# Kernel optimization log

Measured on AMD Instinct MI355X. Metric: run time of the kernel, lower is better.

Reference implementation:

```python
import jax, jax.numpy as jnp
import numpy as np
from math import factorial

# (mul, l, parity) per irrep; parity +1 = even (e), -1 = odd (o)
IRREPS_IN  = [(64, 0, 1), (32, 1, -1), (16, 2, 1)]
IRREPS_OUT = [(64, 0, 1), (32, 1, -1), (16, 2, 1)]
B = 20000


def _su2_cg(j1, m1, j2, m2, j3, m3):
    # Standard SU(2) Clebsch-Gordan coefficient <j1 m1 j2 m2 | j3 m3> (integer j).
    if m3 != m1 + m2:
        return 0.0
    vmin = max(-j1 + j2 + m3, -j1 + m1, 0)
    vmax = min(j2 + j3 + m1, j3 - j1 + j2, j3 + m3)
    if vmax < vmin:
        return 0.0
    f = factorial
    C = ((2 * j3 + 1) * f(j3 + j1 - j2) * f(j3 - j1 + j2) * f(j1 + j2 - j3)
         * f(j3 + m3) * f(j3 - m3)
         / (f(j1 + j2 + j3 + 1) * f(j1 - m1) * f(j1 + m1) * f(j2 - m2) * f(j2 + m2))) ** 0.5
    S = 0.0
    for v in range(vmin, vmax + 1):
        S += ((-1.0) ** (v + j2 + m2) * f(j2 + j3 + m1 - v) * f(j1 - m1 + v)
              / (f(v) * f(j3 - j1 + j2 - v) * f(j3 + m3 - v) * f(v + j1 - j2 - m3)))
    return C * S


def _q(l):
    # Real -> complex spherical-harmonics change of basis, phased so real CG is real (e3nn convention).
    q = np.zeros((2 * l + 1, 2 * l + 1), dtype=np.complex128)
    for m in range(-l, 0):
        q[l + m, l + abs(m)] = 2 ** -0.5
        q[l + m, l - abs(m)] = -1j * 2 ** -0.5
    q[l, l] = 1.0
    for m in range(1, l + 1):
        q[l + m, l + abs(m)] = (-1) ** m * 2 ** -0.5
        q[l + m, l - abs(m)] = 1j * (-1) ** m * 2 ** -0.5
    return (-1j) ** l * q


def _clebsch_gordan(l1, l2, l3):
    # Real-basis CG coefficients, shape (2l1+1, 2l2+1, 2l3+1).
    C = np.zeros((2 * l1 + 1, 2 * l2 + 1, 2 * l3 + 1), dtype=np.complex128)
    for m1 in range(-l1, l1 + 1):
        for m2 in range(-l2, l2 + 1):
            for m3 in range(-l3, l3 + 1):
                C[l1 + m1, l2 + m2, l3 + m3] = _su2_cg(l1, m1, l2, m2, l3, m3)
    Q1, Q2, Q3 = _q(l1), _q(l2), _q(l3)
    Cr = np.einsum('ij,kl,mn,ikn->jlm', Q1, Q2, np.conj(Q3.T), C)
    return np.real(Cr)


def _build():
    # Enumerate all allowed 'uvw' CG paths (i1, i2, i_out); one learned weight per path.
    ins, cgs = [], []
    for i1, (m1, l1, p1) in enumerate(IRREPS_IN):
        for i2, (m2, l2, p2) in enumerate(IRREPS_IN):
            for lo in range(abs(l1 - l2), l1 + l2 + 1):
                po = p1 * p2
                for io, (mo, l3, p3) in enumerate(IRREPS_OUT):
                    if l3 == lo and p3 == po:
                        ins.append((i1, i2, io, (m1, m2, mo)))
                        # 'component' normalization: scale so each output component has unit variance per path
                        cgs.append((_clebsch_gordan(l1, l2, l3) * (2 * l3 + 1) ** 0.5).astype(np.float32))
                        break
    fan = {}
    for (i1, i2, io, (m1, m2, mo)) in ins:
        fan[io] = fan.get(io, 0) + m1 * m2
    alphas = [1.0 / float(np.sqrt(fan[io])) for (_, _, io, _) in ins]
    return ins, cgs, alphas


INSTRUCTIONS, CGS, ALPHAS = _build()  # 11 instructions for these irreps
DIM_IN = sum(m * (2 * l + 1) for m, l, _ in IRREPS_IN)


def setup_inputs() -> dict:
    key = jax.random.key(0)
    keys = jax.random.split(key, 1 + len(INSTRUCTIONS))
    inp = {"x": jax.random.normal(keys[0], (B, DIM_IN), dtype=jnp.float32)}
    for i, (ins, k) in enumerate(zip(INSTRUCTIONS, keys[1:])):
        inp[f"w{i}"] = jax.random.normal(k, ins[3], dtype=jnp.float32)
    return inp


def _tensor_square(x, ws):
    b = x.shape[0]
    xs, off = [], 0
    for m, l, _ in IRREPS_IN:
        d = m * (2 * l + 1)
        xs.append(x[:, off:off + d].reshape(b, m, 2 * l + 1))
        off += d
    outs = [jnp.zeros((b, m, 2 * l + 1), x.dtype) for m, l, _ in IRREPS_OUT]
    for (i1, i2, io, _), w, C, a in zip(INSTRUCTIONS, ws, CGS, ALPHAS):
        # per-path weighted CG contraction: out[b,w,k] = sum_{u,v,i,j} W[u,v,w] C[i,j,k] x[b,u,i] x[b,v,j]
        contrib = jnp.einsum('uvw,ijk,bui,bvj->bwk', w, jnp.asarray(C, x.dtype),
                             xs[i1], xs[i2], optimize='optimal')
        outs[io] = outs[io] + jnp.asarray(a, x.dtype) * contrib
    return jnp.concatenate([o.reshape(b, -1) for o in outs], axis=1)


def reference(x, w0, w1, w2, w3, w4, w5, w6, w7, w8, w9, w10):
    return _tensor_square(x, (w0, w1, w2, w3, w4, w5, w6, w7, w8, w9, w10))
```

## Files before the change

kernel.cpp:

```cpp
#include <hip/hip_runtime.h>
#include <stdint.h>
#include <stddef.h>


namespace cg {

struct Cx { double re, im; };
constexpr Cx cmul(Cx a, Cx b){ return { a.re*b.re - a.im*b.im, a.re*b.im + a.im*b.re }; }

constexpr double fact(int n){ double r = 1.0; for (int i = 2; i <= n; ++i) r *= (double)i; return r; }

constexpr double csqrt(double x){
  if (x <= 0.0) return 0.0;
  double r = x > 1.0 ? x : 1.0;
  for (int i = 0; i < 50; ++i) r = 0.5*(r + x/r);
  return r;
}

constexpr double neg1pow(int k){ return (k % 2 == 0) ? 1.0 : -1.0; }

constexpr double su2_cg(int j1,int m1,int j2,int m2,int j3,int m3){
  if (m3 != m1 + m2) return 0.0;
  int vmin = -j1 + j2 + m3;
  if (-j1 + m1 > vmin) vmin = -j1 + m1;
  if (0 > vmin) vmin = 0;
  int vmax = j2 + j3 + m1;
  if (j3 - j1 + j2 < vmax) vmax = j3 - j1 + j2;
  if (j3 + m3 < vmax) vmax = j3 + m3;
  if (vmax < vmin) return 0.0;
  double C = csqrt((2.0*j3 + 1.0)*fact(j3+j1-j2)*fact(j3-j1+j2)*fact(j1+j2-j3)
                   *fact(j3+m3)*fact(j3-m3)
                   /(fact(j1+j2+j3+1)*fact(j1-m1)*fact(j1+m1)*fact(j2-m2)*fact(j2+m2)));
  double S = 0.0;
  for (int v = vmin; v <= vmax; ++v)
    S += neg1pow(v + j2 + m2)*fact(j2+j3+m1-v)*fact(j1-m1+v)
       /(fact(v)*fact(j3-j1+j2-v)*fact(j3+m3-v)*fact(v+j1-j2-m3));
  return C*S;
}

struct QM { Cx v[5][5]; };
constexpr QM qmat(int l){
  QM q{};
  const double r2 = 0.70710678118654752440;
  for (int m = -l; m < 0; ++m){
    q.v[l+m][l-m] = Cx{ r2, 0.0 };
    q.v[l+m][l+m] = Cx{ 0.0, -r2 };
  }
  q.v[l][l] = Cx{ 1.0, 0.0 };
  for (int m = 1; m <= l; ++m){
    double s = neg1pow(m)*r2;
    q.v[l+m][l+m] = Cx{ s, 0.0 };
    q.v[l+m][l-m] = Cx{ 0.0, s };
  }
  Cx ph = (l % 4 == 0) ? Cx{1,0} : (l % 4 == 1) ? Cx{0,-1} : (l % 4 == 2) ? Cx{-1,0} : Cx{0,1};
  QM out{};
  for (int i = 0; i < 5; ++i) for (int j = 0; j < 5; ++j) out.v[i][j] = cmul(ph, q.v[i][j]);
  return out;
}

struct CGT { double v[5][5][5]; };
constexpr CGT cg_tab(int l1,int l2,int l3){
  double C[5][5][5] = {};
  for (int m1 = -l1; m1 <= l1; ++m1)
    for (int m2 = -l2; m2 <= l2; ++m2)
      for (int m3 = -l3; m3 <= l3; ++m3)
        C[l1+m1][l2+m2][l3+m3] = su2_cg(l1,m1,l2,m2,l3,m3);
  QM Q1 = qmat(l1), Q2 = qmat(l2), Q3 = qmat(l3);
  const int n1 = 2*l1+1, n2 = 2*l2+1, n3 = 2*l3+1;
  const double norm = csqrt(2.0*l3 + 1.0);
  CGT R{};
  for (int j = 0; j < n1; ++j)
    for (int l = 0; l < n2; ++l)
      for (int m = 0; m < n3; ++m){
        Cx s{0,0};
        for (int i = 0; i < n1; ++i)
          for (int k = 0; k < n2; ++k)
            for (int n = 0; n < n3; ++n){
              double c = C[i][k][n];
              if (c != 0.0){
                Cx q3c{ Q3.v[n][m].re, -Q3.v[n][m].im };
                Cx t = cmul(cmul(Q1.v[i][j], Q2.v[k][l]), q3c);
                s.re += t.re*c; s.im += t.im*c;
              }
            }
        R.v[j][l][m] = s.re * norm;
      }
  return R;
}

constexpr double tab_sumsq(const CGT& t, int n1, int n2, int n3){
  double s = 0;
  for (int i = 0; i < n1; ++i) for (int j = 0; j < n2; ++j) for (int k = 0; k < n3; ++k)
    s += t.v[i][j][k]*t.v[i][j][k];
  return s;
}

}

constexpr cg::CGT T121 = cg::cg_tab(1,2,1);
constexpr cg::CGT T211 = cg::cg_tab(2,1,1);
constexpr cg::CGT T112 = cg::cg_tab(1,1,2);
constexpr cg::CGT T222 = cg::cg_tab(2,2,2);
constexpr double C000 = cg::cg_tab(0,0,0).v[0][0][0];
constexpr double C011 = cg::cg_tab(0,1,1).v[0][0][0];
constexpr double C022 = cg::cg_tab(0,2,2).v[0][0][0];
constexpr double C101 = cg::cg_tab(1,0,1).v[0][0][0];
constexpr double C110 = cg::cg_tab(1,1,0).v[0][0][0];
constexpr double C220 = cg::cg_tab(2,2,0).v[0][0][0];
constexpr double C202 = cg::cg_tab(2,0,2).v[0][0][0];

static_assert(C000 > 0.99 && C000 < 1.01, "C000");
static_assert(C011 > 1.72 && C011 < 1.74, "C011");
static_assert(C101 > 1.72 && C101 < 1.74, "C101");
static_assert(C022 > 2.22 && C022 < 2.25, "C022");
static_assert(C202 > 2.22 && C202 < 2.25, "C202");
static_assert(C110*C110 > 0.332 && C110*C110 < 0.334, "C110");
static_assert(C220*C220 > 0.199 && C220*C220 < 0.201, "C220");
static_assert(cg::tab_sumsq(T121,3,5,3) > 8.9  && cg::tab_sumsq(T121,3,5,3) < 9.1,  "T121");
static_assert(cg::tab_sumsq(T211,5,3,3) > 8.9  && cg::tab_sumsq(T211,5,3,3) < 9.1,  "T211");
static_assert(cg::tab_sumsq(T112,3,3,5) > 24.9 && cg::tab_sumsq(T112,3,3,5) < 25.1, "T112");
static_assert(cg::tab_sumsq(T222,5,5,5) > 24.9 && cg::tab_sumsq(T222,5,5,5) < 25.1, "T222");

constexpr double A0 = 1.0/cg::csqrt(5376.0);
constexpr double A1 = 1.0/cg::csqrt(5120.0);
constexpr double A2 = 1.0/cg::csqrt(3328.0);

constexpr double S000 = A0*C000, S110 = A0*C110, S220 = A0*C220;
constexpr double S011 = A1*C011, S101 = A1*C101, S121 = A1, S211 = A1;
constexpr double S022 = A2*C022, S112 = A2,      S202 = A2*C202, S222 = A2;

constexpr int K0 = 5376, K1 = 5120, K2 = 3328;
constexpr int WT1_OFF = 64*K0;
constexpr int WT2_OFF = WT1_OFF + 32*K1;

using short8  = __attribute__((ext_vector_type(8))) short;
using float4v = __attribute__((ext_vector_type(4))) float;

__device__ __forceinline__ unsigned pkbf(float lo, float hi){
  unsigned a = __builtin_bit_cast(unsigned, lo);
  unsigned b = __builtin_bit_cast(unsigned, hi);
  return __builtin_amdgcn_perm(b, a, 0x07060302u);
}

__device__ __forceinline__ short8 mkfrag(const float* s){
  union { short8 v; unsigned u[4]; } f;
  f.u[0] = pkbf(s[0], s[1]);
  f.u[1] = pkbf(s[2], s[3]);
  f.u[2] = pkbf(s[4], s[5]);
  f.u[3] = pkbf(s[6], s[7]);
  return f.v;
}

__device__ __forceinline__ short8 ldB(const unsigned short* p){
  return *reinterpret_cast<const short8*>(p);
}

__device__ __forceinline__ float4v MFMA(short8 a, short8 b, float4v c){
  return __builtin_amdgcn_mfma_f32_16x16x32_bf16(a, b, c, 0, 0, 0);
}

__device__ __forceinline__ unsigned short f2bf_rne(float f){
  unsigned u = __builtin_bit_cast(unsigned, f);
  u += 0x7fffu + ((u >> 16) & 1u);
  return (unsigned short)(u >> 16);
}

#define NZ(c) ((c) > 1e-12 || (c) < -1e-12)

constexpr int XS = 244;

__global__ __launch_bounds__(256)
void tsq_prep(const float* __restrict__ w0, const float* __restrict__ w1,
              const float* __restrict__ w2, const float* __restrict__ w3,
              const float* __restrict__ w4, const float* __restrict__ w5,
              const float* __restrict__ w6, const float* __restrict__ w7,
              const float* __restrict__ w8, const float* __restrict__ w9,
              const float* __restrict__ w10, unsigned short* __restrict__ wt){
  const int s   = blockIdx.x;
  const int g   = blockIdx.y;
  const int tid = threadIdx.x;

  const int lw  = 6 - g;
  const int Wn  = 1 << lw;
  const int NT  = Wn >> 4;
  int Smax;
  unsigned short* obase;
  if (g == 0){ Smax = 168; obase = wt; }
  else if (g == 1){ Smax = 160; obase = wt + WT1_OFF; }
  else { Smax = 104; obase = wt + WT2_OFF; }
  if (s >= Smax) return;

  __shared__ unsigned short tl[32*66];
  const int st = Wn + 2;

  const int nel = 32 << lw;
  for (int idx = tid; idx < nel; idx += 256){
    const int kk = idx >> lw, n = idx & (Wn - 1);
    const int k  = s*32 + kk;
    float v;
    if (g == 0){
      if (k < 4096)       v = w0[k*64 + n] * (float)S000;
      else if (k < 5120)  v = w4[(k-4096)*64 + n] * (float)S110;
      else                v = w9[(k-5120)*64 + n] * (float)S220;
    } else if (g == 1){
      if (k < 2048){
        const int u = k & 63, vv = k >> 6;
        v = w1[(u*32 + vv)*32 + n] * (float)S011;
      } else if (k < 4096){
        v = w3[(k-2048)*32 + n] * (float)S101;
      } else if (k < 4608){
        const int kl = k - 4096; const int u = kl & 31, vv = kl >> 5;
        v = w6[(u*16 + vv)*32 + n] * (float)S121;
      } else {
        v = w8[(k-4608)*32 + n] * (float)S211;
      }
    } else {
      if (k < 1024){
        const int u = k & 63, vv = k >> 6;
        v = w2[(u*16 + vv)*16 + n] * (float)S022;
      } else if (k < 2048){
        v = w5[(k-1024)*16 + n] * (float)S112;
      } else if (k < 3072){
        v = w7[(k-2048)*16 + n] * (float)S202;
      } else {
        v = w10[(k-3072)*16 + n] * (float)S222;
      }
    }
    tl[kk*st + n] = f2bf_rne(v);
  }
  __syncthreads();

  unsigned short* o = obase + (size_t)s*NT*512;
  const int nout = NT*512;
  for (int idx = tid; idx < nout; idx += 256){
    const int nt  = idx >> 9;
    const int r   = idx & 511;
    const int col = r >> 5;
    const int kk  = r & 31;
    o[idx] = tl[kk*st + nt*16 + col];
  }
}

__global__ __launch_bounds__(512, 4)
void tsq_main(const float* __restrict__ x, const unsigned short* __restrict__ wt,
              float* __restrict__ out){
  __shared__ float lx[64*XS];
  const int g    = blockIdx.x;
  const int b0   = blockIdx.y * 64;
  const int tid  = threadIdx.x;
  const int wv   = tid >> 6;
  const int lane = tid & 63;
  const int col  = lane & 15;
  const int tg   = lane >> 4;
  const int fo   = col*32 + tg*8;

  for (int i = tid; i < 64*60; i += 512){
    const int r = i / 60, c = i - r*60;
    int gb = b0 + r; if (gb > 19999) gb = 19999;
    const float4 v = *(reinterpret_cast<const float4*>(x + (size_t)gb*240) + c);
    *reinterpret_cast<float4*>(&lx[r*XS + c*4]) = v;
  }
  __syncthreads();

  const float4v z4 = {0.f, 0.f, 0.f, 0.f};

  if (g == 0){
    const unsigned short* bpl = wt + fo;
    const int mh  = wv >> 2;
    const int kh  = wv & 3;
    const int par = kh & 1;

    float4v acc[2][4];
    #pragma unroll
    for (int mt = 0; mt < 2; ++mt)
      #pragma unroll
      for (int nt = 0; nt < 4; ++nt) acc[mt][nt] = z4;

    const float* rbase[2];
    #pragma unroll
    for (int mt = 0; mt < 2; ++mt) rbase[mt] = &lx[(mh*32 + mt*16 + col)*XS];

    float w8a[2][8];
    #pragma unroll
    for (int mt = 0; mt < 2; ++mt){
      const float4 v0 = *reinterpret_cast<const float4*>(rbase[mt] + par*32 + tg*8);
      const float4 v1 = *reinterpret_cast<const float4*>(rbase[mt] + par*32 + tg*8 + 4);
      w8a[mt][0]=v0.x; w8a[mt][1]=v0.y; w8a[mt][2]=v0.z; w8a[mt][3]=v0.w;
      w8a[mt][4]=v1.x; w8a[mt][5]=v1.y; w8a[mt][6]=v1.z; w8a[mt][7]=v1.w;
    }

    #pragma unroll 2
    for (int s = kh; s < 128; s += 4){
      short8 bf[4];
      #pragma unroll
      for (int nt = 0; nt < 4; ++nt) bf[nt] = ldB(bpl + (s*4 + nt)*512);
      const int u = s >> 1;
      #pragma unroll
      for (int mt = 0; mt < 2; ++mt){
        const float xu = rbase[mt][u];
        float sv[8];
        #pragma unroll
        for (int t = 0; t < 8; ++t) sv[t] = xu * w8a[mt][t];
        const short8 af = mkfrag(sv);
        #pragma unroll
        for (int nt = 0; nt < 4; ++nt) acc[mt][nt] = MFMA(af, bf[nt], acc[mt][nt]);
      }
    }
    float x1w[2][24];
    #pragma unroll
    for (int mt = 0; mt < 2; ++mt)
      #pragma unroll
      for (int q = 0; q < 6; ++q){
        const float4 v = *reinterpret_cast<const float4*>(rbase[mt] + 64 + tg*24 + q*4);
        x1w[mt][q*4+0] = v.x; x1w[mt][q*4+1] = v.y;
        x1w[mt][q*4+2] = v.z; x1w[mt][q*4+3] = v.w;
      }
    #pragma unroll 2
    for (int s = 128 + kh; s < 160; s += 4){
      short8 bf[4];
      #pragma unroll
      for (int nt = 0; nt < 4; ++nt) bf[nt] = ldB(bpl + (s*4 + nt)*512);
      const int u = s - 128;
      #pragma unroll
      for (int mt = 0; mt < 2; ++mt){
        const float* rb = rbase[mt];
        const float u0 = rb[64+u*3], u1 = rb[64+u*3+1], u2 = rb[64+u*3+2];
        float sv[8];
        #pragma unroll
        for (int t = 0; t < 8; ++t)
          sv[t] = fmaf(u0, x1w[mt][t*3], fmaf(u1, x1w[mt][t*3+1], u2*x1w[mt][t*3+2]));
        const short8 af = mkfrag(sv);
        #pragma unroll
        for (int nt = 0; nt < 4; ++nt) acc[mt][nt] = MFMA(af, bf[nt], acc[mt][nt]);
      }
    }
    for (int s = 160 + kh; s < 168; s += 4){
      short8 bf[4];
      #pragma unroll
      for (int nt = 0; nt < 4; ++nt) bf[nt] = ldB(bpl + (s*4 + nt)*512);
      const int ub = (s - 160)*2 + (tg >> 1);
      #pragma unroll
      for (int mt = 0; mt < 2; ++mt){
        const float* rb = rbase[mt];
        float xu[5];
        #pragma unroll
        for (int i = 0; i < 5; ++i) xu[i] = rb[160 + ub*5 + i];
        float xv[40];
        #pragma unroll
        for (int q = 0; q < 10; ++q){
          const float4 v = *reinterpret_cast<const float4*>(rb + 160 + (tg&1)*40 + q*4);
          xv[q*4+0] = v.x; xv[q*4+1] = v.y; xv[q*4+2] = v.z; xv[q*4+3] = v.w;
        }
        float sv[8];
        #pragma unroll
        for (int t = 0; t < 8; ++t){
          float a = 0.f;
          #pragma unroll
          for (int i = 0; i < 5; ++i) a = fmaf(xu[i], xv[t*5+i], a);
          sv[t] = a;
        }
        const short8 af = mkfrag(sv);
        #pragma unroll
        for (int nt = 0; nt < 4; ++nt) acc[mt][nt] = MFMA(af, bf[nt], acc[mt][nt]);
      }
    }
    __syncthreads();
    float* red = lx;
    if (kh != 0){
      #pragma unroll
      for (int mt = 0; mt < 2; ++mt)
        #pragma unroll
        for (int nt = 0; nt < 4; ++nt)
          #pragma unroll
          for (int r = 0; r < 4; ++r)
            red[mh*6144 + ((kh-1)*8 + mt*4 + nt)*256 + (tg*4 + r)*16 + col] = acc[mt][nt][r];
    }
    __syncthreads();
    if (kh == 0){
      #pragma unroll
      for (int mt = 0; mt < 2; ++mt)
        #pragma unroll
        for (int r = 0; r < 4; ++r){
          const int b = b0 + mh*32 + mt*16 + tg*4 + r;
          if (b < 20000){
            #pragma unroll
            for (int nt = 0; nt < 4; ++nt){
              float v = acc[mt][nt][r];
              #pragma unroll
              for (int w2 = 1; w2 < 4; ++w2)
                v += red[mh*6144 + ((w2-1)*8 + mt*4 + nt)*256 + (tg*4 + r)*16 + col];
              out[(size_t)b*240 + nt*16 + col] = v;
            }
          }
        }
    }

  } else if (g == 1){
    const unsigned short* bpl = wt + WT1_OFF + fo;
    const int mq = wv >> 1;
    const int kh = wv & 1;
    const float* rb = &lx[(mq*16 + col)*XS];

    float4v acc[3][2];
    #pragma unroll
    for (int k3 = 0; k3 < 3; ++k3)
      #pragma unroll
      for (int nt = 0; nt < 2; ++nt) acc[k3][nt] = z4;

    float w8[8];
    {
      const float4 v0 = *reinterpret_cast<const float4*>(rb + kh*32 + tg*8);
      const float4 v1 = *reinterpret_cast<const float4*>(rb + kh*32 + tg*8 + 4);
      w8[0]=v0.x; w8[1]=v0.y; w8[2]=v0.z; w8[3]=v0.w;
      w8[4]=v1.x; w8[5]=v1.y; w8[6]=v1.z; w8[7]=v1.w;
    }
    float x1w[24];
    #pragma unroll
    for (int q = 0; q < 6; ++q){
      const float4 v = *reinterpret_cast<const float4*>(rb + 64 + tg*24 + q*4);
      x1w[q*4+0] = v.x; x1w[q*4+1] = v.y; x1w[q*4+2] = v.z; x1w[q*4+3] = v.w;
    }

    #pragma unroll 2
    for (int s = kh; s < 128; s += 2){
      const short8 bf0 = ldB(bpl + (s*2    )*512);
      const short8 bf1 = ldB(bpl + (s*2 + 1)*512);
      const int m = (s >> 1) & 31;
      const float c0 = rb[64+m*3], c1 = rb[64+m*3+1], c2 = rb[64+m*3+2];
      float sv0[8], sv1[8], sv2[8];
      #pragma unroll
      for (int t = 0; t < 8; ++t){
        const float xw = w8[t];
        sv0[t] = xw*c0; sv1[t] = xw*c1; sv2[t] = xw*c2;
      }
      const short8 a0 = mkfrag(sv0), a1 = mkfrag(sv1), a2 = mkfrag(sv2);
      acc[0][0] = MFMA(a0, bf0, acc[0][0]);
      acc[0][1] = MFMA(a0, bf1, acc[0][1]);
      acc[1][0] = MFMA(a1, bf0, acc[1][0]);
      acc[1][1] = MFMA(a1, bf1, acc[1][1]);
      acc[2][0] = MFMA(a2, bf0, acc[2][0]);
      acc[2][1] = MFMA(a2, bf1, acc[2][1]);
    }
    for (int s = 128 + kh; s < 144; s += 2){
      const short8 bf0 = ldB(bpl + (s*2    )*512);
      const short8 bf1 = ldB(bpl + (s*2 + 1)*512);
      const int v2 = s - 128;
      float xq[5];
      #pragma unroll
      for (int j = 0; j < 5; ++j) xq[j] = rb[160 + v2*5 + j];
      float sv0[8], sv1[8], sv2[8];
      #pragma unroll
      for (int t = 0; t < 8; ++t){
        float s3[3] = {0.f, 0.f, 0.f};
        #pragma unroll
        for (int i = 0; i < 3; ++i){
          const float ai = x1w[t*3 + i];
          #pragma unroll
          for (int j = 0; j < 5; ++j){
            const float p = ai * xq[j];
            #pragma unroll
            for (int kk = 0; kk < 3; ++kk){
              const double cd = T121.v[i][j][kk];
              if (NZ(cd)) s3[kk] = fmaf((float)cd, p, s3[kk]);
            }
          }
        }
        sv0[t] = s3[0]; sv1[t] = s3[1]; sv2[t] = s3[2];
      }
      const short8 a0 = mkfrag(sv0), a1 = mkfrag(sv1), a2 = mkfrag(sv2);
      acc[0][0] = MFMA(a0, bf0, acc[0][0]);
      acc[0][1] = MFMA(a0, bf1, acc[0][1]);
      acc[1][0] = MFMA(a1, bf0, acc[1][0]);
      acc[1][1] = MFMA(a1, bf1, acc[1][1]);
      acc[2][0] = MFMA(a2, bf0, acc[2][0]);
      acc[2][1] = MFMA(a2, bf1, acc[2][1]);
    }
    for (int s = 144 + kh; s < 160; s += 2){
      const short8 bf0 = ldB(bpl + (s*2    )*512);
      const short8 bf1 = ldB(bpl + (s*2 + 1)*512);
      const int u2 = s - 144;
      float xq[5];
      #pragma unroll
      for (int i = 0; i < 5; ++i) xq[i] = rb[160 + u2*5 + i];
      float sv0[8], sv1[8], sv2[8];
      #pragma unroll
      for (int t = 0; t < 8; ++t){
        float s3[3] = {0.f, 0.f, 0.f};
        #pragma unroll
        for (int j = 0; j < 3; ++j){
          const float aj = x1w[t*3 + j];
          #pragma unroll
          for (int i = 0; i < 5; ++i){
            const float p = xq[i] * aj;
            #pragma unroll
            for (int kk = 0; kk < 3; ++kk){
              const double cd = T211.v[i][j][kk];
              if (NZ(cd)) s3[kk] = fmaf((float)cd, p, s3[kk]);
            }
          }
        }
        sv0[t] = s3[0]; sv1[t] = s3[1]; sv2[t] = s3[2];
      }
      const short8 a0 = mkfrag(sv0), a1 = mkfrag(sv1), a2 = mkfrag(sv2);
      acc[0][0] = MFMA(a0, bf0, acc[0][0]);
      acc[0][1] = MFMA(a0, bf1, acc[0][1]);
      acc[1][0] = MFMA(a1, bf0, acc[1][0]);
      acc[1][1] = MFMA(a1, bf1, acc[1][1]);
      acc[2][0] = MFMA(a2, bf0, acc[2][0]);
      acc[2][1] = MFMA(a2, bf1, acc[2][1]);
    }
    __syncthreads();
    float* red = lx;
    if (kh == 1){
      #pragma unroll
      for (int k3 = 0; k3 < 3; ++k3)
        #pragma unroll
        for (int nt = 0; nt < 2; ++nt)
          #pragma unroll
          for (int r = 0; r < 4; ++r)
            red[mq*1536 + (k3*2 + nt)*256 + (tg*4 + r)*16 + col] = acc[k3][nt][r];
    }
    __syncthreads();
    if (kh == 0){
      #pragma unroll
      for (int r = 0; r < 4; ++r){
        const int b = b0 + mq*16 + tg*4 + r;
        if (b < 20000){
          #pragma unroll
          for (int nt = 0; nt < 2; ++nt){
            const int w2 = nt*16 + col;
            float* o = out + (size_t)b*240 + 64 + 3*w2;
            #pragma unroll
            for (int k3 = 0; k3 < 3; ++k3)
              o[k3] = acc[k3][nt][r]
                    + red[mq*1536 + (k3*2 + nt)*256 + (tg*4 + r)*16 + col];
          }
        }
      }
    }

  } else {
    const unsigned short* bpl = wt + WT2_OFF + fo;
    const int mq = wv >> 1;
    const int kh = wv & 1;
    const float* rb = &lx[(mq*16 + col)*XS];

    float4v acc[5] = { z4, z4, z4, z4, z4 };

    float w8[8];
    {
      const float4 v0 = *reinterpret_cast<const float4*>(rb + kh*32 + tg*8);
      const float4 v1 = *reinterpret_cast<const float4*>(rb + kh*32 + tg*8 + 4);
      w8[0]=v0.x; w8[1]=v0.y; w8[2]=v0.z; w8[3]=v0.w;
      w8[4]=v1.x; w8[5]=v1.y; w8[6]=v1.z; w8[7]=v1.w;
    }
    float x1w[24];
    #pragma unroll
    for (int q = 0; q < 6; ++q){
      const float4 v = *reinterpret_cast<const float4*>(rb + 64 + tg*24 + q*4);
      x1w[q*4+0] = v.x; x1w[q*4+1] = v.y; x1w[q*4+2] = v.z; x1w[q*4+3] = v.w;
    }

    #pragma unroll 2
    for (int s = kh; s < 32; s += 2){
      const short8 bf = ldB(bpl + s*512);
      const int v2 = s >> 1;
      float xq[5];
      #pragma unroll
      for (int j = 0; j < 5; ++j) xq[j] = rb[160 + v2*5 + j];
      float sv[5][8];
      #pragma unroll
      for (int t = 0; t < 8; ++t){
        const float xw = w8[t];
        #pragma unroll
        for (int k5 = 0; k5 < 5; ++k5) sv[k5][t] = xw * xq[k5];
      }
      #pragma unroll
      for (int k5 = 0; k5 < 5; ++k5) acc[k5] = MFMA(mkfrag(sv[k5]), bf, acc[k5]);
    }
    #pragma unroll 2
    for (int s = 32 + kh; s < 64; s += 2){
      const short8 bf = ldB(bpl + s*512);
      const int u = s - 32;
      float xu[3];
      #pragma unroll
      for (int i = 0; i < 3; ++i) xu[i] = rb[64 + u*3 + i];
      float sv[5][8];
      #pragma unroll
      for (int t = 0; t < 8; ++t){
        float s5[5] = {0.f,0.f,0.f,0.f,0.f};
        #pragma unroll
        for (int i = 0; i < 3; ++i)
          #pragma unroll
          for (int j = 0; j < 3; ++j){
            const float p = xu[i] * x1w[t*3 + j];
            #pragma unroll
            for (int kk = 0; kk < 5; ++kk){
              const double cd = T112.v[i][j][kk];
              if (NZ(cd)) s5[kk] = fmaf((float)cd, p, s5[kk]);
            }
          }
        #pragma unroll
        for (int kk = 0; kk < 5; ++kk) sv[kk][t] = s5[kk];
      }
      #pragma unroll
      for (int k5 = 0; k5 < 5; ++k5) acc[k5] = MFMA(mkfrag(sv[k5]), bf, acc[k5]);
    }
    #pragma unroll 2
    for (int s = 64 + kh; s < 96; s += 2){
      const short8 bf = ldB(bpl + s*512);
      const int u2 = (s - 64) >> 1;
      float xq[5];
      #pragma unroll
      for (int i = 0; i < 5; ++i) xq[i] = rb[160 + u2*5 + i];
      float sv[5][8];
      #pragma unroll
      for (int t = 0; t < 8; ++t){
        const float xw = w8[t];
        #pragma unroll
        for (int k5 = 0; k5 < 5; ++k5) sv[k5][t] = xq[k5] * xw;
      }
      #pragma unroll
      for (int k5 = 0; k5 < 5; ++k5) acc[k5] = MFMA(mkfrag(sv[k5]), bf, acc[k5]);
    }
    float x2w[40];
    #pragma unroll
    for (int q = 0; q < 10; ++q){
      const float4 v = *reinterpret_cast<const float4*>(rb + 160 + (tg&1)*40 + q*4);
      x2w[q*4+0] = v.x; x2w[q*4+1] = v.y; x2w[q*4+2] = v.z; x2w[q*4+3] = v.w;
    }
    #pragma unroll 1
    for (int s = 96 + kh; s < 104; s += 2){
      const short8 bf = ldB(bpl + s*512);
      const int ub = (s - 96)*2 + (tg >> 1);
      float xu[5];
      #pragma unroll
      for (int i = 0; i < 5; ++i) xu[i] = rb[160 + ub*5 + i];
      float sv[5][8];
      #pragma unroll
      for (int t = 0; t < 8; ++t){
        float s5[5] = {0.f,0.f,0.f,0.f,0.f};
        #pragma unroll
        for (int i = 0; i < 5; ++i)
          #pragma unroll
          for (int j = 0; j < 5; ++j){
            const float p = xu[i] * x2w[t*5 + j];
            #pragma unroll
            for (int kk = 0; kk < 5; ++kk){
              const double cd = T222.v[i][j][kk];
              if (NZ(cd)) s5[kk] = fmaf((float)cd, p, s5[kk]);
            }
          }
        #pragma unroll
        for (int kk = 0; kk < 5; ++kk) sv[kk][t] = s5[kk];
      }
      #pragma unroll
      for (int k5 = 0; k5 < 5; ++k5) acc[k5] = MFMA(mkfrag(sv[k5]), bf, acc[k5]);
    }
    __syncthreads();
    float* red = lx;
    if (kh == 1){
      #pragma unroll
      for (int k5 = 0; k5 < 5; ++k5)
        #pragma unroll
        for (int r = 0; r < 4; ++r)
          red[mq*1280 + k5*256 + (tg*4 + r)*16 + col] = acc[k5][r];
    }
    __syncthreads();
    if (kh == 0){
      #pragma unroll
      for (int r = 0; r < 4; ++r){
        const int b = b0 + mq*16 + tg*4 + r;
        if (b < 20000){
          float* o = out + (size_t)b*240 + 160 + 5*col;
          #pragma unroll
          for (int k5 = 0; k5 < 5; ++k5)
            o[k5] = acc[k5][r] + red[mq*1280 + k5*256 + (tg*4 + r)*16 + col];
        }
      }
    }
  }
}

extern "C" void kernel_launch(void* const* d_in, const int* in_sizes, int n_in,
                              void* d_out, int out_size, void* d_ws, size_t ws_size,
                              hipStream_t stream){
  (void)in_sizes; (void)n_in; (void)out_size; (void)ws_size;
  const float* x = (const float*)d_in[0];
  const float* w[11];
  for (int i = 0; i < 11; ++i) w[i] = (const float*)d_in[1 + i];
  unsigned short* wt = (unsigned short*)d_ws;
  float* out = (float*)d_out;

  dim3 gp(168, 3);
  tsq_prep<<<gp, 256, 0, stream>>>(w[0], w[1], w[2], w[3], w[4], w[5],
                                   w[6], w[7], w[8], w[9], w[10], wt);
  dim3 gm(3, 313);
  tsq_main<<<gm, 512, 0, stream>>>(x, wt, out);
}
```

Measured before the change: 188.5 us.

## Fold symmetric tensor-square paths into shared weights to shrink GEMM K

Exploits the symmetry x_u⊗x_v = x_v⊗x_u: the prep kernel sums weights of mirrored paths (w0 upper/lower triangle, w1+w3, w6+w8 via T211=T121^T, w2+w7), so the main kernel's reduction dimension shrinks in all three output groups. The l=0 path now covers only the upper triangle of u,v blocks. It also refactors the CG contractions to precompute a per-step partial (x_u contracted with C) before the per-lane products, which cuts VALU work. Removing unroll pragmas and adding a static_assert for the transpose identity come along with it. Bf16 rounding now applies to summed weights, which slightly changes numerics.

Result: faster. 167.8 us (-11.0%).

```diff
diff --git a/kernel.cpp b/kernel.cpp
--- a/kernel.cpp
+++ b/kernel.cpp
@@ -121,6 +121,19 @@
 static_assert(cg::tab_sumsq(T112,3,3,5) > 24.9 && cg::tab_sumsq(T112,3,3,5) < 25.1, "T112");
 static_assert(cg::tab_sumsq(T222,5,5,5) > 24.9 && cg::tab_sumsq(T222,5,5,5) < 25.1, "T222");
 
+constexpr double t121_t211_swapdiff(){
+  double m = 0;
+  for (int i = 0; i < 5; ++i)
+    for (int j = 0; j < 3; ++j)
+      for (int k = 0; k < 3; ++k){
+        double d = T211.v[i][j][k] - T121.v[j][i][k];
+        if (d < 0) d = -d;
+        if (d > m) m = d;
+      }
+  return m;
+}
+static_assert(t121_t211_swapdiff() < 1e-9, "T211 != T121^T -- fold invalid");
+
 constexpr double A0 = 1.0/cg::csqrt(5376.0);
 constexpr double A1 = 1.0/cg::csqrt(5120.0);
 constexpr double A2 = 1.0/cg::csqrt(3328.0);
@@ -129,7 +142,7 @@
 constexpr double S011 = A1*C011, S101 = A1*C101, S121 = A1, S211 = A1;
 constexpr double S022 = A2*C022, S112 = A2,      S202 = A2*C202, S222 = A2;
 
-constexpr int K0 = 5376, K1 = 5120, K2 = 3328;
+constexpr int K0 = 4352, K1 = 2560, K2 = 2304;
 constexpr int WT1_OFF = 64*K0;
 constexpr int WT2_OFF = WT1_OFF + 32*K1;
 
@@ -185,9 +198,9 @@
   const int NT  = Wn >> 4;
   int Smax;
   unsigned short* obase;
-  if (g == 0){ Smax = 168; obase = wt; }
-  else if (g == 1){ Smax = 160; obase = wt + WT1_OFF; }
-  else { Smax = 104; obase = wt + WT2_OFF; }
+  if (g == 0){ Smax = 136; obase = wt; }
+  else if (g == 1){ Smax = 80; obase = wt + WT1_OFF; }
+  else { Smax = 72; obase = wt + WT2_OFF; }
   if (s >= Smax) return;
 
   __shared__ unsigned short tl[32*66];
@@ -196,34 +209,41 @@
   const int nel = 32 << lw;
   for (int idx = tid; idx < nel; idx += 256){
     const int kk = idx >> lw, n = idx & (Wn - 1);
-    const int k  = s*32 + kk;
     float v;
     if (g == 0){
-      if (k < 4096)       v = w0[k*64 + n] * (float)S000;
-      else if (k < 5120)  v = w4[(k-4096)*64 + n] * (float)S110;
-      else                v = w9[(k-5120)*64 + n] * (float)S220;
+      if (s < 64){
+        const int u = s >> 1, vv = (s & 1)*32 + kk;
+        v = w0[(u*64 + vv)*64 + n];
+        if (s & 1) v += w0[(vv*64 + u)*64 + n];
+        v *= (float)S000;
+      } else if (s < 96){
+        const int u = s - 32, vv = 32 + kk;
+        v = w0[(u*64 + vv)*64 + n] * (float)S000;
+      } else if (s < 128){
+        v = w4[((s-96)*32 + kk)*64 + n] * (float)S110;
+      } else {
+        v = w9[((s-128)*32 + kk)*64 + n] * (float)S220;
+      }
     } else if (g == 1){
-      if (k < 2048){
-        const int u = k & 63, vv = k >> 6;
-        v = w1[(u*32 + vv)*32 + n] * (float)S011;
-      } else if (k < 4096){
-        v = w3[(k-2048)*32 + n] * (float)S101;
-      } else if (k < 4608){
-        const int kl = k - 4096; const int u = kl & 31, vv = kl >> 5;
-        v = w6[(u*16 + vv)*32 + n] * (float)S121;
+      const int k = s*32 + kk;
+      if (s < 64){
+        v = w1[((k&63)*32 + (k>>6))*32 + n] * (float)S011
+          + w3[k*32 + n] * (float)S101;
       } else {
-        v = w8[(k-4608)*32 + n] * (float)S211;
+        const int kr = k - 2048;
+        const int u1 = kr & 31, v2 = kr >> 5;
+        v = w6[(u1*16 + v2)*32 + n] * (float)S121
+          + w8[(v2*32 + u1)*32 + n] * (float)S211;
       }
     } else {
-      if (k < 1024){
-        const int u = k & 63, vv = k >> 6;
-        v = w2[(u*16 + vv)*16 + n] * (float)S022;
-      } else if (k < 2048){
+      const int k = s*32 + kk;
+      if (s < 32){
+        v = w2[((k&63)*16 + (k>>6))*16 + n] * (float)S022
+          + w7[k*16 + n] * (float)S202;
+      } else if (s < 64){
         v = w5[(k-1024)*16 + n] * (float)S112;
-      } else if (k < 3072){
-        v = w7[(k-2048)*16 + n] * (float)S202;
       } else {
-        v = w10[(k-3072)*16 + n] * (float)S222;
+        v = w10[(k-2048)*16 + n] * (float)S222;
       }
     }
     tl[kk*st + n] = f2bf_rne(v);
@@ -280,17 +300,20 @@
     #pragma unroll
     for (int mt = 0; mt < 2; ++mt) rbase[mt] = &lx[(mh*32 + mt*16 + col)*XS];
 
-    float w8a[2][8];
+    float wA[2][8], wB[2][8];
     #pragma unroll
     for (int mt = 0; mt < 2; ++mt){
-      const float4 v0 = *reinterpret_cast<const float4*>(rbase[mt] + par*32 + tg*8);
-      const float4 v1 = *reinterpret_cast<const float4*>(rbase[mt] + par*32 + tg*8 + 4);
-      w8a[mt][0]=v0.x; w8a[mt][1]=v0.y; w8a[mt][2]=v0.z; w8a[mt][3]=v0.w;
-      w8a[mt][4]=v1.x; w8a[mt][5]=v1.y; w8a[mt][6]=v1.z; w8a[mt][7]=v1.w;
-    }
-
-    #pragma unroll 2
-    for (int s = kh; s < 128; s += 4){
+      const float4 a0 = *reinterpret_cast<const float4*>(rbase[mt] + par*32 + tg*8);
+      const float4 a1 = *reinterpret_cast<const float4*>(rbase[mt] + par*32 + tg*8 + 4);
+      wA[mt][0]=a0.x; wA[mt][1]=a0.y; wA[mt][2]=a0.z; wA[mt][3]=a0.w;
+      wA[mt][4]=a1.x; wA[mt][5]=a1.y; wA[mt][6]=a1.z; wA[mt][7]=a1.w;
+      const float4 b0v = *reinterpret_cast<const float4*>(rbase[mt] + 32 + tg*8);
+      const float4 b1v = *reinterpret_cast<const float4*>(rbase[mt] + 32 + tg*8 + 4);
+      wB[mt][0]=b0v.x; wB[mt][1]=b0v.y; wB[mt][2]=b0v.z; wB[mt][3]=b0v.w;
+      wB[mt][4]=b1v.x; wB[mt][5]=b1v.y; wB[mt][6]=b1v.z; wB[mt][7]=b1v.w;
+    }
+
+    for (int s = kh; s < 64; s += 4){
       short8 bf[4];
       #pragma unroll
       for (int nt = 0; nt < 4; ++nt) bf[nt] = ldB(bpl + (s*4 + nt)*512);
@@ -300,7 +323,23 @@
         const float xu = rbase[mt][u];
         float sv[8];
         #pragma unroll
-        for (int t = 0; t < 8; ++t) sv[t] = xu * w8a[mt][t];
+        for (int t = 0; t < 8; ++t) sv[t] = xu * wA[mt][t];
+        const short8 af = mkfrag(sv);
+        #pragma unroll
+        for (int nt = 0; nt < 4; ++nt) acc[mt][nt] = MFMA(af, bf[nt], acc[mt][nt]);
+      }
+    }
+    for (int s = 64 + kh; s < 96; s += 4){
+      short8 bf[4];
+      #pragma unroll
+      for (int nt = 0; nt < 4; ++nt) bf[nt] = ldB(bpl + (s*4 + nt)*512);
+      const int u = s - 32;
+      #pragma unroll
+      for (int mt = 0; mt < 2; ++mt){
+        const float xu = rbase[mt][u];
+        float sv[8];
+        #pragma unroll
+        for (int t = 0; t < 8; ++t) sv[t] = xu * wB[mt][t];
         const short8 af = mkfrag(sv);
         #pragma unroll
         for (int nt = 0; nt < 4; ++nt) acc[mt][nt] = MFMA(af, bf[nt], acc[mt][nt]);
@@ -315,12 +354,11 @@
         x1w[mt][q*4+0] = v.x; x1w[mt][q*4+1] = v.y;
         x1w[mt][q*4+2] = v.z; x1w[mt][q*4+3] = v.w;
       }
-    #pragma unroll 2
-    for (int s = 128 + kh; s < 160; s += 4){
+    for (int s = 96 + kh; s < 128; s += 4){
       short8 bf[4];
       #pragma unroll
       for (int nt = 0; nt < 4; ++nt) bf[nt] = ldB(bpl + (s*4 + nt)*512);
-      const int u = s - 128;
+      const int u = s - 96;
       #pragma unroll
       for (int mt = 0; mt < 2; ++mt){
         const float* rb = rbase[mt];
@@ -334,11 +372,11 @@
         for (int nt = 0; nt < 4; ++nt) acc[mt][nt] = MFMA(af, bf[nt], acc[mt][nt]);
       }
     }
-    for (int s = 160 + kh; s < 168; s += 4){
+    for (int s = 128 + kh; s < 136; s += 4){
       short8 bf[4];
       #pragma unroll
       for (int nt = 0; nt < 4; ++nt) bf[nt] = ldB(bpl + (s*4 + nt)*512);
-      const int ub = (s - 160)*2 + (tg >> 1);
+      const int ub = (s - 128)*2 + (tg >> 1);
       #pragma unroll
       for (int mt = 0; mt < 2; ++mt){
         const float* rb = rbase[mt];
@@ -421,11 +459,10 @@
       x1w[q*4+0] = v.x; x1w[q*4+1] = v.y; x1w[q*4+2] = v.z; x1w[q*4+3] = v.w;
     }
 
-    #pragma unroll 2
-    for (int s = kh; s < 128; s += 2){
+    for (int s = kh; s < 64; s += 2){
       const short8 bf0 = ldB(bpl + (s*2    )*512);
       const short8 bf1 = ldB(bpl + (s*2 + 1)*512);
-      const int m = (s >> 1) & 31;
+      const int m = s >> 1;
       const float c0 = rb[64+m*3], c1 = rb[64+m*3+1], c2 = rb[64+m*3+2];
       float sv0[8], sv1[8], sv2[8];
       #pragma unroll
@@ -441,65 +478,33 @@
       acc[2][0] = MFMA(a2, bf0, acc[2][0]);
       acc[2][1] = MFMA(a2, bf1, acc[2][1]);
     }
-    for (int s = 128 + kh; s < 144; s += 2){
+    for (int s = 64 + kh; s < 80; s += 2){
       const short8 bf0 = ldB(bpl + (s*2    )*512);
       const short8 bf1 = ldB(bpl + (s*2 + 1)*512);
-      const int v2 = s - 128;
+      const int v2 = s - 64;
       float xq[5];
       #pragma unroll
       for (int j = 0; j < 5; ++j) xq[j] = rb[160 + v2*5 + j];
+      float t3[3][3];
+      #pragma unroll
+      for (int kk = 0; kk < 3; ++kk)
+        #pragma unroll
+        for (int i = 0; i < 3; ++i){
+          float a = 0.f;
+          #pragma unroll
+          for (int j = 0; j < 5; ++j){
+            const double cd = T121.v[i][j][kk];
+            if (NZ(cd)) a = fmaf((float)cd, xq[j], a);
+          }
+          t3[kk][i] = a;
+        }
       float sv0[8], sv1[8], sv2[8];
       #pragma unroll
       for (int t = 0; t < 8; ++t){
-        float s3[3] = {0.f, 0.f, 0.f};
-        #pragma unroll
-        for (int i = 0; i < 3; ++i){
-          const float ai = x1w[t*3 + i];
-          #pragma unroll
-          for (int j = 0; j < 5; ++j){
-            const float p = ai * xq[j];
-            #pragma unroll
-            for (int kk = 0; kk < 3; ++kk){
-              const double cd = T121.v[i][j][kk];
-              if (NZ(cd)) s3[kk] = fmaf((float)cd, p, s3[kk]);
-            }
-          }
-        }
-        sv0[t] = s3[0]; sv1[t] = s3[1]; sv2[t] = s3[2];
-      }
-      const short8 a0 = mkfrag(sv0), a1 = mkfrag(sv1), a2 = mkfrag(sv2);
-      acc[0][0] = MFMA(a0, bf0, acc[0][0]);
-      acc[0][1] = MFMA(a0, bf1, acc[0][1]);
-      acc[1][0] = MFMA(a1, bf0, acc[1][0]);
-      acc[1][1] = MFMA(a1, bf1, acc[1][1]);
-      acc[2][0] = MFMA(a2, bf0, acc[2][0]);
-      acc[2][1] = MFMA(a2, bf1, acc[2][1]);
-    }
-    for (int s = 144 + kh; s < 160; s += 2){
-      const short8 bf0 = ldB(bpl + (s*2    )*512);
-      const short8 bf1 = ldB(bpl + (s*2 + 1)*512);
-      const int u2 = s - 144;
-      float xq[5];
-      #pragma unroll
-      for (int i = 0; i < 5; ++i) xq[i] = rb[160 + u2*5 + i];
-      float sv0[8], sv1[8], sv2[8];
-      #pragma unroll
-      for (int t = 0; t < 8; ++t){
-        float s3[3] = {0.f, 0.f, 0.f};
-        #pragma unroll
-        for (int j = 0; j < 3; ++j){
-          const float aj = x1w[t*3 + j];
-          #pragma unroll
-          for (int i = 0; i < 5; ++i){
-            const float p = xq[i] * aj;
-            #pragma unroll
-            for (int kk = 0; kk < 3; ++kk){
-              const double cd = T211.v[i][j][kk];
-              if (NZ(cd)) s3[kk] = fmaf((float)cd, p, s3[kk]);
-            }
-          }
-        }
-        sv0[t] = s3[0]; sv1[t] = s3[1]; sv2[t] = s3[2];
+        const float a0_ = x1w[t*3], a1_ = x1w[t*3+1], a2_ = x1w[t*3+2];
+        sv0[t] = fmaf(a0_, t3[0][0], fmaf(a1_, t3[0][1], a2_*t3[0][2]));
+        sv1[t] = fmaf(a0_, t3[1][0], fmaf(a1_, t3[1][1], a2_*t3[1][2]));
+        sv2[t] = fmaf(a0_, t3[2][0], fmaf(a1_, t3[2][1], a2_*t3[2][2]));
       }
       const short8 a0 = mkfrag(sv0), a1 = mkfrag(sv1), a2 = mkfrag(sv2);
       acc[0][0] = MFMA(a0, bf0, acc[0][0]);
@@ -561,7 +566,6 @@
       x1w[q*4+0] = v.x; x1w[q*4+1] = v.y; x1w[q*4+2] = v.z; x1w[q*4+3] = v.w;
     }
 
-    #pragma unroll 2
     for (int s = kh; s < 32; s += 2){
       const short8 bf = ldB(bpl + s*512);
       const int v2 = s >> 1;
@@ -578,47 +582,32 @@
       #pragma unroll
       for (int k5 = 0; k5 < 5; ++k5) acc[k5] = MFMA(mkfrag(sv[k5]), bf, acc[k5]);
     }
-    #pragma unroll 2
     for (int s = 32 + kh; s < 64; s += 2){
       const short8 bf = ldB(bpl + s*512);
       const int u = s - 32;
       float xu[3];
       #pragma unroll
       for (int i = 0; i < 3; ++i) xu[i] = rb[64 + u*3 + i];
+      float t5[5][3];
+      #pragma unroll
+      for (int kk = 0; kk < 5; ++kk)
+        #pragma unroll
+        for (int j = 0; j < 3; ++j){
+          float a = 0.f;
+          #pragma unroll
+          for (int i = 0; i < 3; ++i){
+            const double cd = T112.v[i][j][kk];
+            if (NZ(cd)) a = fmaf((float)cd, xu[i], a);
+          }
+          t5[kk][j] = a;
+        }
       float sv[5][8];
       #pragma unroll
       for (int t = 0; t < 8; ++t){
-        float s5[5] = {0.f,0.f,0.f,0.f,0.f};
-        #pragma unroll
-        for (int i = 0; i < 3; ++i)
-          #pragma unroll
-          for (int j = 0; j < 3; ++j){
-            const float p = xu[i] * x1w[t*3 + j];
-            #pragma unroll
-            for (int kk = 0; kk < 5; ++kk){
-              const double cd = T112.v[i][j][kk];
-              if (NZ(cd)) s5[kk] = fmaf((float)cd, p, s5[kk]);
-            }
-          }
-        #pragma unroll
-        for (int kk = 0; kk < 5; ++kk) sv[kk][t] = s5[kk];
-      }
-      #pragma unroll
-      for (int k5 = 0; k5 < 5; ++k5) acc[k5] = MFMA(mkfrag(sv[k5]), bf, acc[k5]);
-    }
-    #pragma unroll 2
-    for (int s = 64 + kh; s < 96; s += 2){
-      const short8 bf = ldB(bpl + s*512);
-      const int u2 = (s - 64) >> 1;
-      float xq[5];
-      #pragma unroll
-      for (int i = 0; i < 5; ++i) xq[i] = rb[160 + u2*5 + i];
-      float sv[5][8];
-      #pragma unroll
-      for (int t = 0; t < 8; ++t){
-        const float xw = w8[t];
-        #pragma unroll
-        for (int k5 = 0; k5 < 5; ++k5) sv[k5][t] = xq[k5] * xw;
+        const float b0_ = x1w[t*3], b1_ = x1w[t*3+1], b2_ = x1w[t*3+2];
+        #pragma unroll
+        for (int kk = 0; kk < 5; ++kk)
+          sv[kk][t] = fmaf(b0_, t5[kk][0], fmaf(b1_, t5[kk][1], b2_*t5[kk][2]));
       }
       #pragma unroll
       for (int k5 = 0; k5 < 5; ++k5) acc[k5] = MFMA(mkfrag(sv[k5]), bf, acc[k5]);
@@ -629,30 +618,35 @@
       const float4 v = *reinterpret_cast<const float4*>(rb + 160 + (tg&1)*40 + q*4);
       x2w[q*4+0] = v.x; x2w[q*4+1] = v.y; x2w[q*4+2] = v.z; x2w[q*4+3] = v.w;
     }
-    #pragma unroll 1
-    for (int s = 96 + kh; s < 104; s += 2){
+    for (int s = 64 + kh; s < 72; s += 2){
       const short8 bf = ldB(bpl + s*512);
-      const int ub = (s - 96)*2 + (tg >> 1);
+      const int ub = (s - 64)*2 + (tg >> 1);
       float xu[5];
       #pragma unroll
       for (int i = 0; i < 5; ++i) xu[i] = rb[160 + ub*5 + i];
+      float t5[5][5];
+      #pragma unroll
+      for (int kk = 0; kk < 5; ++kk)
+        #pragma unroll
+        for (int j = 0; j < 5; ++j){
+          float a = 0.f;
+          #pragma unroll
+          for (int i = 0; i < 5; ++i){
+            const double cd = T222.v[i][j][kk];
+            if (NZ(cd)) a = fmaf((float)cd, xu[i], a);
+          }
+          t5[kk][j] = a;
+        }
       float sv[5][8];
       #pragma unroll
       for (int t = 0; t < 8; ++t){
-        float s5[5] = {0.f,0.f,0.f,0.f,0.f};
-        #pragma unroll
-        for (int i = 0; i < 5; ++i)
-          #pragma unroll
-          for (int j = 0; j < 5; ++j){
-            const float p = xu[i] * x2w[t*5 + j];
-            #pragma unroll
-            for (int kk = 0; kk < 5; ++kk){
-              const double cd = T222.v[i][j][kk];
-              if (NZ(cd)) s5[kk] = fmaf((float)cd, p, s5[kk]);
-            }
-          }
-        #pragma unroll
-        for (int kk = 0; kk < 5; ++kk) sv[kk][t] = s5[kk];
+        #pragma unroll
+        for (int kk = 0; kk < 5; ++kk){
+          float a = 0.f;
+          #pragma unroll
+          for (int j = 0; j < 5; ++j) a = fmaf(x2w[t*5+j], t5[kk][j], a);
+          sv[kk][t] = a;
+        }
       }
       #pragma unroll
       for (int k5 = 0; k5 < 5; ++k5) acc[k5] = MFMA(mkfrag(sv[k5]), bf, acc[k5]);
@@ -692,7 +686,7 @@
   unsigned short* wt = (unsigned short*)d_ws;
   float* out = (float*)d_out;
 
-  dim3 gp(168, 3);
+  dim3 gp(136, 3);
   tsq_prep<<<gp, 256, 0, stream>>>(w[0], w[1], w[2], w[3], w[4], w[5],
                                    w[6], w[7], w[8], w[9], w[10], wt);
   dim3 gm(3, 313);
```
